# Kernel optimization log

Hardware: AMD Instinct MI355X
Metric: run time of the kernel (lower is better)

## Reference

```python
import jax, jax.numpy as jnp
import numpy as np

B, S, D = 2, 2048, 2048
H, HK, HD = 16, 4, 128          # query heads, kv heads, head dim (H*HD == D)
HID = 4 * D                      # SwiGLU hidden (mult=4)
WIN, SINK = 1024, 4              # sliding window, attention sink tokens
EPS = 1e-6
ROPE_BASE = 10000.0


def rmsnorm(x, g):
    return x * jax.lax.rsqrt(jnp.mean(x * x, axis=-1, keepdims=True) + EPS) * g


def rope_tables(seq_len, head_dim):
    inv = 1.0 / (ROPE_BASE ** (jnp.arange(0, head_dim, 2, dtype=jnp.float32) / head_dim))
    ang = jnp.arange(seq_len, dtype=jnp.float32)[:, None] * inv[None, :]  # [S, HD/2]
    return jnp.cos(ang), jnp.sin(ang)


def apply_rope(x, cos, sin):
    # x: [B, S, h, HD]; rotate-half convention
    x1, x2 = jnp.split(x, 2, axis=-1)
    c = cos[None, :, None, :]
    s = sin[None, :, None, :]
    return jnp.concatenate([x1 * c - x2 * s, x2 * c + x1 * s], axis=-1)


def setup_inputs() -> dict:
    key = jax.random.key(0)
    ks = jax.random.split(key, 10)
    p = 0.02
    return {
        "x": jax.random.normal(ks[0], (B, S, D), dtype=jnp.float32),
        "g1": jnp.ones((D,), dtype=jnp.float32),
        "g2": jnp.ones((D,), dtype=jnp.float32),
        "wq": jax.random.normal(ks[1], (D, H * HD), dtype=jnp.float32) * p,
        "wk": jax.random.normal(ks[2], (D, HK * HD), dtype=jnp.float32) * p,
        "wv": jax.random.normal(ks[3], (D, HK * HD), dtype=jnp.float32) * p,
        "wo": jax.random.normal(ks[4], (H * HD, D), dtype=jnp.float32) * p,
        "w_gate": jax.random.normal(ks[5], (D, HID), dtype=jnp.float32) * p,
        "w_up": jax.random.normal(ks[6], (D, HID), dtype=jnp.float32) * p,
        "w_down": jax.random.normal(ks[7], (HID, D), dtype=jnp.float32) * p,
    }


def reference(x, g1, g2, wq, wk, wv, wo, w_gate, w_up, w_down):
    # ---- pre-norm attention ----
    h = rmsnorm(x, g1)
    q = (h @ wq).reshape(B, S, H, HD)
    k = (h @ wk).reshape(B, S, HK, HD)
    v = (h @ wv).reshape(B, S, HK, HD)

    cos, sin = rope_tables(S, HD)
    q = apply_rope(q, cos, sin)
    k = apply_rope(k, cos, sin)

    # GQA: expand kv heads to query heads
    rep = H // HK
    k = jnp.repeat(k, rep, axis=2)  # [B, S, H, HD]
    v = jnp.repeat(v, rep, axis=2)

    scores = jnp.einsum("bqhd,bkhd->bhqk", q, k) / jnp.sqrt(jnp.float32(HD))

    # causal + sliding-window + attention-sink mask
    i = jnp.arange(S)[:, None]
    j = jnp.arange(S)[None, :]
    allowed = (j <= i) & (((i - j) < WIN) | (j < SINK))  # [S, S]
    scores = jnp.where(allowed[None, None], scores, jnp.float32(-1e9))

    attn = jax.nn.softmax(scores, axis=-1)
    a = jnp.einsum("bhqk,bkhd->bqhd", attn, v).reshape(B, S, H * HD) @ wo

    x = x + a

    # ---- pre-norm SwiGLU FFN ----
    h2 = rmsnorm(x, g2)
    ffn = (jax.nn.silu(h2 @ w_gate) * (h2 @ w_up)) @ w_down
    return x + ffn
```

## Files before the change

### kernel.cpp

```cpp
#include <hip/hip_runtime.h>
#include <hip/hip_bf16.h>
#include <stdint.h>

#define TOK 4096
#define SEQ 2048
#define DM 2048
#define NH 16
#define NKV 4
#define HDIM 128
#define HID 8192
#define WIN 1024
#define SINKN 4

typedef float f32x4 __attribute__((ext_vector_type(4)));
typedef __bf16 bf16x8 __attribute__((ext_vector_type(8)));
typedef unsigned short u16;
typedef unsigned int u32;

#define VM(n) asm volatile("s_waitcnt vmcnt(" #n ")" ::: "memory")
#define LGKM0 asm volatile("s_waitcnt lgkmcnt(0)" ::: "memory")

__device__ __forceinline__ u16 f2bf(float f) {
  union { float f; u32 u; } v; v.f = f;
  return (u16)((v.u + 0x7fffu + ((v.u >> 16) & 1u)) >> 16);
}
__device__ __forceinline__ float bf2f(u16 h) {
  union { u32 u; float f; } v; v.u = ((u32)h) << 16;
  return v.f;
}
__device__ __forceinline__ f32x4 mfma16(bf16x8 a, bf16x8 b, f32x4 c) {
  return __builtin_amdgcn_mfma_f32_16x16x32_bf16(a, b, c, 0, 0, 0);
}
__device__ __forceinline__ void gld16(const u16* g, u16* l) {
  __builtin_amdgcn_global_load_lds(
      (const __attribute__((address_space(1))) u32*)g,
      (__attribute__((address_space(3))) u32*)l, 16, 0, 0);
}
__device__ __forceinline__ void bar() {
  asm volatile("s_barrier" ::: "memory");
}
__device__ __forceinline__ void swz_rc(int c, int& row, int& k8) {
  row = 2 * (c >> 3) + (((c >> 2) & 1) ^ ((c >> 4) & 1));
  k8 = (c & 3) ^ (row & 3);
}
__device__ __forceinline__ void raster8(int wg, int nwg, int nbx, int& bx, int& by) {
  int cpx = nwg >> 3;
  int s = (wg & 7) * cpx + (wg >> 3);
  by = 8 * (s / (8 * nbx)) + (s & 7);
  bx = (s >> 3) % nbx;
}

__global__ __launch_bounds__(256)
void wtrans(const float* __restrict__ in, u16* __restrict__ out, int K, int N)
{
  __shared__ float t[32][33];
  int tx = threadIdx.x & 31, ty = threadIdx.x >> 5;
  int bx = blockIdx.x, by = blockIdx.y;
  #pragma unroll
  for (int i = 0; i < 4; i++) {
    int r = ty + i * 8;
    t[r][tx] = in[(size_t)(by * 32 + r) * N + bx * 32 + tx];
  }
  __syncthreads();
  #pragma unroll
  for (int i = 0; i < 4; i++) {
    int r = ty + i * 8;
    out[(size_t)(bx * 32 + r) * K + by * 32 + tx] = f2bf(t[tx][r]);
  }
}

__global__ __launch_bounds__(256)
void vtrans(const u16* __restrict__ in, int ld, u16* __restrict__ out)
{
  __shared__ u16 t[32][33];
  int tx = threadIdx.x & 31, ty = threadIdx.x >> 5;
  int bx = blockIdx.x;
  int by = blockIdx.y;
  #pragma unroll
  for (int i = 0; i < 4; i++) {
    int r = ty + i * 8;
    t[r][tx] = in[(size_t)(by * 32 + r) * ld + bx * 32 + tx];
  }
  __syncthreads();
  int b = (by * 32) >> 11;
  int s0 = (by * 32) & (SEQ - 1);
  #pragma unroll
  for (int i = 0; i < 4; i++) {
    int c = bx * 32 + ty + i * 8;
    out[(size_t)(b * (NKV * HDIM) + c) * SEQ + s0 + tx] = t[tx][ty + i * 8];
  }
}

__global__ __launch_bounds__(256)
void rope_table_k(float* __restrict__ ct, float* __restrict__ st)
{
  int idx = blockIdx.x * 256 + threadIdx.x;
  int pos = idx >> 6, d = idx & 63;
  float inv = powf(10000.0f, -(float)d / 64.0f);
  float a = (float)pos * inv;
  ct[idx] = cosf(a);
  st[idx] = sinf(a);
}

__global__ void rope_apply_k(u16* __restrict__ q, int ld,
                             const float* __restrict__ ct,
                             const float* __restrict__ st, float scale)
{
  int t = blockIdx.x;
  int hh = threadIdx.x >> 6;
  int d = threadIdx.x & 63;
  int pos = t & (SEQ - 1);
  size_t base = (size_t)t * ld + hh * HDIM + d;
  float x1 = bf2f(q[base]), x2 = bf2f(q[base + 64]);
  float c = ct[pos * 64 + d], s = st[pos * 64 + d];
  q[base]      = f2bf((x1 * c - x2 * s) * scale);
  q[base + 64] = f2bf((x2 * c + x1 * s) * scale);
}

__global__ __launch_bounds__(256)
void rmsnorm_k(const float* __restrict__ x, const float* __restrict__ g,
               u16* __restrict__ o)
{
  int row = blockIdx.x;
  int tid = threadIdx.x;
  const float* xr = x + (size_t)row * DM;
  float4 v0 = *(const float4*)(xr + tid * 8);
  float4 v1 = *(const float4*)(xr + tid * 8 + 4);
  float ss = v0.x*v0.x + v0.y*v0.y + v0.z*v0.z + v0.w*v0.w
           + v1.x*v1.x + v1.y*v1.y + v1.z*v1.z + v1.w*v1.w;
  #pragma unroll
  for (int d = 1; d < 64; d <<= 1) ss += __shfl_xor(ss, d);
  __shared__ float red[4];
  if ((tid & 63) == 0) red[tid >> 6] = ss;
  __syncthreads();
  float inv = rsqrtf((red[0] + red[1] + red[2] + red[3]) * (1.0f / DM) + 1e-6f);
  float4 g0 = *(const float4*)(g + tid * 8);
  float4 g1 = *(const float4*)(g + tid * 8 + 4);
  ushort4 o0, o1;
  o0.x = f2bf(v0.x * inv * g0.x); o0.y = f2bf(v0.y * inv * g0.y);
  o0.z = f2bf(v0.z * inv * g0.z); o0.w = f2bf(v0.w * inv * g0.w);
  o1.x = f2bf(v1.x * inv * g1.x); o1.y = f2bf(v1.y * inv * g1.y);
  o1.z = f2bf(v1.z * inv * g1.z); o1.w = f2bf(v1.w * inv * g1.w);
  *(ushort4*)(o + (size_t)row * DM + tid * 8) = o0;
  *(ushort4*)(o + (size_t)row * DM + tid * 8 + 4) = o1;
}

template<int EPI, int GU>
__global__ __launch_bounds__(512, 1)
void gemmp(const u16* __restrict__ A, const u16* __restrict__ Bt,
           const u16* __restrict__ Bu, u16* __restrict__ Cb,
           float* __restrict__ Cf, const float* __restrict__ X,
           int M, int N, int K, int nbx)
{
  constexpr int ASZ = 128 * 64;
  constexpr int SLOT = ASZ + 256 * 64;
  __shared__ u16 lds[3 * SLOT];

  int bx, by;
  raster8(blockIdx.x, gridDim.x, nbx, bx, by);
  int m0 = by * 128;
  int n0 = bx * (GU ? 128 : 256);

  int tid = threadIdx.x;
  int l = tid & 63, w = tid >> 6;
  int l16 = l & 15, lg = l >> 4;
  int wr = w >> 2, wc = w & 3;

  int aoff[4][2], boff[4][2];
  #pragma unroll
  for (int m = 0; m < 4; m++)
    #pragma unroll
    for (int kk = 0; kk < 2; kk++) {
      int row = wr * 64 + m * 16 + l16;
      aoff[m][kk] = ((row * 128 + kk * 64 + lg * 16) ^ ((row & 7) << 4)) >> 1;
    }
  #pragma unroll
  for (int n = 0; n < 4; n++)
    #pragma unroll
    for (int kk = 0; kk < 2; kk++) {
      int br = GU ? ((n >> 1) * 128 + wc * 32 + (n & 1) * 16 + l16)
                  : (wc * 64 + n * 16 + l16);
      boff[n][kk] = ASZ + (((br * 128 + kk * 64 + lg * 16) ^ ((br & 7) << 4)) >> 1);
    }

  int urow = tid >> 3;
  int cc = (tid & 7) ^ (urow & 7);
  const u16* pA[2];
  const u16* pB[4];
  pA[0] = A + (size_t)(m0 + urow) * K + cc * 8;
  pA[1] = A + (size_t)(m0 + 64 + urow) * K + cc * 8;
  #pragma unroll
  for (int u = 0; u < 4; u++) {
    if (GU) pB[u] = (u < 2 ? Bt + (size_t)(n0 + u * 64 + urow) * K
                           : Bu + (size_t)(n0 + (u - 2) * 64 + urow) * K) + cc * 8;
    else    pB[u] = Bt + (size_t)(n0 + u * 64 + urow) * K + cc * 8;
  }

  const int NT = K >> 6;

  auto stA = [&](int tt, int u) {
    gld16(pA[u] + (size_t)tt * 64, lds + (tt % 3) * SLOT + u * 4096 + tid * 8);
  };
  auto stB = [&](int tt, int u) {
    gld16(pB[u] + (size_t)tt * 64, lds + (tt % 3) * SLOT + ASZ + u * 4096 + tid * 8);
  };

  #pragma unroll
  for (int u = 0; u < 4; u++) stB(0, u);
  stA(0, 0); stA(0, 1);
  #pragma unroll
  for (int u = 0; u < 4; u++) stB(1, u);
  stA(1, 0); stA(1, 1);
  VM(6);
  bar();

  f32x4 acc[4][4];
  f32x4 zero = {0.f, 0.f, 0.f, 0.f};
  #pragma unroll
  for (int m = 0; m < 4; m++)
    #pragma unroll
    for (int n = 0; n < 4; n++) acc[m][n] = zero;

  for (int t = 0; t < NT; ++t) {
    u16* cur = lds + (t % 3) * SLOT;
    const bool st = (t + 2 < NT);

    if (st) { stB(t + 2, 0); stB(t + 2, 1); stB(t + 2, 2); }
    bf16x8 a[4][2], b[2][2];
    #pragma unroll
    for (int m = 0; m < 4; m++) {
      a[m][0] = *(const bf16x8*)(cur + aoff[m][0]);
      a[m][1] = *(const bf16x8*)(cur + aoff[m][1]);
    }
    #pragma unroll
    for (int n = 0; n < 2; n++) {
      b[n][0] = *(const bf16x8*)(cur + boff[n][0]);
      b[n][1] = *(const bf16x8*)(cur + boff[n][1]);
    }
    bar();
    LGKM0;
    __builtin_amdgcn_sched_barrier(0);
    __builtin_amdgcn_s_setprio(1);
    #pragma unroll
    for (int m = 0; m < 4; m++)
      #pragma unroll
      for (int n = 0; n < 2; n++) {
        acc[m][n] = mfma16(a[m][0], b[n][0], acc[m][n]);
        acc[m][n] = mfma16(a[m][1], b[n][1], acc[m][n]);
      }
    __builtin_amdgcn_s_setprio(0);
    __builtin_amdgcn_sched_barrier(0);
    bar();

    if (st) { stB(t + 2, 3); stA(t + 2, 0); stA(t + 2, 1); }
    bf16x8 c2[2][2];
    #pragma unroll
    for (int n = 0; n < 2; n++) {
      c2[n][0] = *(const bf16x8*)(cur + boff[n + 2][0]);
      c2[n][1] = *(const bf16x8*)(cur + boff[n + 2][1]);
    }
    if (st) { VM(6); }
    else if (t + 1 < NT) { VM(0); }
    bar();
    LGKM0;
    __builtin_amdgcn_sched_barrier(0);
    __builtin_amdgcn_s_setprio(1);
    #pragma unroll
    for (int m = 0; m < 4; m++)
      #pragma unroll
      for (int n = 0; n < 2; n++) {
        acc[m][n + 2] = mfma16(a[m][0], c2[n][0], acc[m][n + 2]);
        acc[m][n + 2] = mfma16(a[m][1], c2[n][1], acc[m][n + 2]);
      }
    __builtin_amdgcn_s_setprio(0);
    __builtin_amdgcn_sched_barrier(0);
    bar();
  }

  if (GU) {
    #pragma unroll
    for (int m = 0; m < 4; m++) {
      int row = m0 + wr * 64 + m * 16 + lg * 4;
      #pragma unroll
      for (int n = 0; n < 2; n++) {
        int col = n0 + wc * 32 + n * 16 + l16;
        #pragma unroll
        for (int r = 0; r < 4; r++) {
          float gt = acc[m][n][r];
          float up = acc[m][n + 2][r];
          float sg = gt / (1.0f + __expf(-gt));
          Cb[(size_t)(row + r) * N + col] = f2bf(sg * up);
        }
      }
    }
  } else {
    #pragma unroll
    for (int m = 0; m < 4; m++) {
      int row = m0 + wr * 64 + m * 16 + lg * 4;
      #pragma unroll
      for (int n = 0; n < 4; n++) {
        int col = n0 + wc * 64 + n * 16 + l16;
        #pragma unroll
        for (int r = 0; r < 4; r++) {
          size_t idx = (size_t)(row + r) * N + col;
          float v = acc[m][n][r];
          if (EPI == 0) {
            Cb[idx] = f2bf(v);
          } else if (EPI == 1) {
            Cf[idx] = X[idx] + v;
          } else {
            Cf[idx] += v;
          }
        }
      }
    }
  }
}

__global__ __launch_bounds__(256)
void attn_k(const u16* __restrict__ qb, int ldq,
            const u16* __restrict__ kb, int ldk,
            const u16* __restrict__ vbt, u16* __restrict__ ao)
{
  int q0 = blockIdx.x * 128;
  int h = blockIdx.y;
  int b = blockIdx.z;
  int hk = h >> 2;
  int tid = threadIdx.x;
  int w = tid >> 6, l = tid & 63;
  int l16 = l & 15, lg = l >> 4;

  __shared__ u16 Ks[32 * 128];
  __shared__ u16 Vt[128 * 32];
  __shared__ u16 Ps[4][32 * 40];
  u16* Pw = Ps[w];

  bf16x8 qf[2][4];
  #pragma unroll
  for (int m = 0; m < 2; m++)
    #pragma unroll
    for (int kd = 0; kd < 4; kd++) {
      int row = q0 + w * 32 + m * 16 + l16;
      qf[m][kd] = *(const bf16x8*)(qb + (size_t)(b * SEQ + row) * ldq
                                   + h * HDIM + kd * 32 + lg * 8);
    }

  f32x4 oacc[2][8];
  float mrun[2][4], lrun[2][4];
  f32x4 zero = {0.f, 0.f, 0.f, 0.f};
  #pragma unroll
  for (int m = 0; m < 2; m++) {
    #pragma unroll
    for (int nd = 0; nd < 8; nd++) oacc[m][nd] = zero;
    #pragma unroll
    for (int r = 0; r < 4; r++) { mrun[m][r] = -1e9f; lrun[m][r] = 0.f; }
  }

  int kr0 = tid >> 4,        kc0 = (tid & 15) ^ (kr0 & 7);
  int kr1 = (tid + 256) >> 4, kc1 = (tid & 15) ^ (kr1 & 7);
  int vd0, vk0, vd1, vk1;
  swz_rc(tid, vd0, vk0);
  swz_rc(tid + 256, vd1, vk1);
  const u16* kbase = kb + (size_t)(b * SEQ) * ldk + hk * HDIM;
  const u16* vbase = vbt + (size_t)(b * NKV + hk) * HDIM * SEQ;

  int koff[2][4];
  #pragma unroll
  for (int n = 0; n < 2; n++)
    #pragma unroll
    for (int kd = 0; kd < 4; kd++) {
      int key = n * 16 + l16;
      koff[n][kd] = ((key * 128) + kd * 32 + lg * 8) ^ ((key & 7) * 8);
    }
  int voff[8];
  #pragma unroll
  for (int nd = 0; nd < 8; nd++) {
    int d = nd * 16 + l16;
    voff[nd] = (d * 32 + lg * 8) ^ ((d & 7) * 8);
  }

  int lo = (q0 >= WIN) ? ((q0 - (WIN - 1)) >> 5) : 0;
  int hi = (q0 + 127) >> 5;

  for (int it = (lo > 0 ? lo - 1 : 0); it <= hi; ++it) {
    int kt = (it < lo) ? 0 : it;
    gld16(kbase + (size_t)(kt * 32 + kr0) * ldk + kc0 * 8, Ks + tid * 8);
    gld16(kbase + (size_t)(kt * 32 + kr1) * ldk + kc1 * 8, Ks + (tid + 256) * 8);
    gld16(vbase + (size_t)vd0 * SEQ + kt * 32 + vk0 * 8, Vt + tid * 8);
    gld16(vbase + (size_t)vd1 * SEQ + kt * 32 + vk1 * 8, Vt + (tid + 256) * 8);
    __syncthreads();

    f32x4 sacc[2][2];
    sacc[0][0] = zero; sacc[0][1] = zero; sacc[1][0] = zero; sacc[1][1] = zero;
    #pragma unroll
    for (int kd = 0; kd < 4; kd++) {
      bf16x8 kf0 = *(const bf16x8*)(Ks + koff[0][kd]);
      bf16x8 kf1 = *(const bf16x8*)(Ks + koff[1][kd]);
      #pragma unroll
      for (int m = 0; m < 2; m++) {
        sacc[m][0] = mfma16(qf[m][kd], kf0, sacc[m][0]);
        sacc[m][1] = mfma16(qf[m][kd], kf1, sacc[m][1]);
      }
    }

    #pragma unroll
    for (int m = 0; m < 2; m++) {
      float sc[4];
      #pragma unroll
      for (int r = 0; r < 4; r++) {
        int i = q0 + w * 32 + m * 16 + lg * 4 + r;
        int j0 = kt * 32 + l16;
        int j1 = j0 + 16;
        float s0 = sacc[m][0][r];
        float s1 = sacc[m][1][r];
        bool ok0 = (j0 <= i) && ((i - j0 < WIN) || (j0 < SINKN));
        bool ok1 = (j1 <= i) && ((i - j1 < WIN) || (j1 < SINKN));
        s0 = ok0 ? s0 : -1e9f;
        s1 = ok1 ? s1 : -1e9f;
        float mx = fmaxf(s0, s1);
        mx = fmaxf(mx, __shfl_xor(mx, 1));
        mx = fmaxf(mx, __shfl_xor(mx, 2));
        mx = fmaxf(mx, __shfl_xor(mx, 4));
        mx = fmaxf(mx, __shfl_xor(mx, 8));
        float mold = mrun[m][r];
        float mnew = fmaxf(mold, mx);
        float scl = __expf(mold - mnew);
        mrun[m][r] = mnew;
        float p0 = __expf(s0 - mnew);
        float p1 = __expf(s1 - mnew);
        int prow = m * 16 + lg * 4 + r;
        Pw[prow * 40 + l16] = f2bf(p0);
        Pw[prow * 40 + 16 + l16] = f2bf(p1);
        float ps = p0 + p1;
        ps += __shfl_xor(ps, 1);
        ps += __shfl_xor(ps, 2);
        ps += __shfl_xor(ps, 4);
        ps += __shfl_xor(ps, 8);
        lrun[m][r] = lrun[m][r] * scl + ps;
        sc[r] = scl;
      }
      #pragma unroll
      for (int nd = 0; nd < 8; nd++) {
        oacc[m][nd][0] *= sc[0];
        oacc[m][nd][1] *= sc[1];
        oacc[m][nd][2] *= sc[2];
        oacc[m][nd][3] *= sc[3];
      }
    }

    bf16x8 pa0 = *(const bf16x8*)(Pw + l16 * 40 + lg * 8);
    bf16x8 pa1 = *(const bf16x8*)(Pw + (16 + l16) * 40 + lg * 8);
    #pragma unroll
    for (int nd = 0; nd < 8; nd++) {
      bf16x8 vf = *(const bf16x8*)(Vt + voff[nd]);
      oacc[0][nd] = mfma16(pa0, vf, oacc[0][nd]);
      oacc[1][nd] = mfma16(pa1, vf, oacc[1][nd]);
    }
    __syncthreads();
  }

  #pragma unroll
  for (int m = 0; m < 2; m++)
    #pragma unroll
    for (int r = 0; r < 4; r++) {
      float invl = 1.0f / lrun[m][r];
      int row = q0 + w * 32 + m * 16 + lg * 4 + r;
      #pragma unroll
      for (int nd = 0; nd < 8; nd++) {
        int col = nd * 16 + l16;
        ao[(size_t)(b * SEQ + row) * (NH * HDIM) + h * HDIM + col] =
            f2bf(oacc[m][nd][r] * invl);
      }
    }
}

extern "C" void kernel_launch(void* const* d_in, const int* in_sizes, int n_in,
                              void* d_out, int out_size, void* d_ws, size_t ws_size,
                              hipStream_t stream)
{
  (void)in_sizes; (void)n_in; (void)out_size;
  const float* x  = (const float*)d_in[0];
  const float* g1 = (const float*)d_in[1];
  const float* g2 = (const float*)d_in[2];
  const float* wq = (const float*)d_in[3];
  const float* wk = (const float*)d_in[4];
  const float* wv = (const float*)d_in[5];
  const float* wo = (const float*)d_in[6];
  const float* wg = (const float*)d_in[7];
  const float* wu = (const float*)d_in[8];
  const float* wd = (const float*)d_in[9];
  float* out = (float*)d_out;

  char* ws = (char*)d_ws;
  size_t off = 0;
  auto alloc = [&](size_t bytes) {
    char* p = ws + off;
    off += (bytes + 255) & ~(size_t)255;
    return p;
  };
  const int NQKV = 3072;
  u16* wqkv_t = (u16*)alloc((size_t)NQKV * DM * 2);
  u16* wo_t   = (u16*)alloc((size_t)DM * DM * 2);
  u16* wg_t   = (u16*)alloc((size_t)HID * DM * 2);
  u16* wu_t   = (u16*)alloc((size_t)HID * DM * 2);
  u16* wd_t   = (u16*)alloc((size_t)DM * HID * 2);
  u16* hb     = (u16*)alloc((size_t)TOK * DM * 2);
  char* span0 = ws + off;
  u16* qkvb   = (u16*)alloc((size_t)TOK * NQKV * 2);
  u16* vbt    = (u16*)alloc((size_t)TOK * NKV * HDIM * 2);
  u16* aob    = (u16*)alloc((size_t)TOK * NH * HDIM * 2);
  size_t span_used = (size_t)(ws + off - span0);
  size_t gu_need = (size_t)TOK * HID * 2;
  if (gu_need > span_used) alloc(gu_need - span_used);
  u16* gu = (u16*)span0;
  float* ct  = (float*)alloc((size_t)SEQ * 64 * 4);
  float* st  = (float*)alloc((size_t)SEQ * 64 * 4);
  if (off > ws_size) return;

  dim3 blk(256);
  dim3 blk512(512);

  wtrans<<<dim3(DM / 32, DM / 32), blk, 0, stream>>>(wq, wqkv_t, DM, DM);
  wtrans<<<dim3((NKV * HDIM) / 32, DM / 32), blk, 0, stream>>>(wk, wqkv_t + (size_t)DM * DM, DM, NKV * HDIM);
  wtrans<<<dim3((NKV * HDIM) / 32, DM / 32), blk, 0, stream>>>(wv, wqkv_t + (size_t)(DM + NKV * HDIM) * DM, DM, NKV * HDIM);
  wtrans<<<dim3(DM / 32, DM / 32), blk, 0, stream>>>(wo, wo_t, DM, DM);
  wtrans<<<dim3(HID / 32, DM / 32), blk, 0, stream>>>(wg, wg_t, DM, HID);
  wtrans<<<dim3(HID / 32, DM / 32), blk, 0, stream>>>(wu, wu_t, DM, HID);
  wtrans<<<dim3(DM / 32, HID / 32), blk, 0, stream>>>(wd, wd_t, HID, DM);

  rope_table_k<<<SEQ * 64 / 256, blk, 0, stream>>>(ct, st);
  rmsnorm_k<<<TOK, blk, 0, stream>>>(x, g1, hb);

  gemmp<0, 0><<<dim3((NQKV / 256) * (TOK / 128)), blk512, 0, stream>>>(
      hb, wqkv_t, nullptr, qkvb, nullptr, nullptr, TOK, NQKV, DM, NQKV / 256);

  rope_apply_k<<<TOK, dim3(NH * 64), 0, stream>>>(qkvb, NQKV, ct, st, 0.08838834764831845f);
  rope_apply_k<<<TOK, dim3(NKV * 64), 0, stream>>>(qkvb + DM, NQKV, ct, st, 1.0f);
  vtrans<<<dim3((NKV * HDIM) / 32, TOK / 32), blk, 0, stream>>>(qkvb + DM + NKV * HDIM, NQKV, vbt);

  attn_k<<<dim3(SEQ / 128, NH, 2), blk, 0, stream>>>(qkvb, NQKV, qkvb + DM, NQKV, vbt, aob);

  gemmp<1, 0><<<dim3((DM / 256) * (TOK / 128)), blk512, 0, stream>>>(
      aob, wo_t, nullptr, nullptr, out, x, TOK, DM, DM, DM / 256);
  rmsnorm_k<<<TOK, blk, 0, stream>>>(out, g2, hb);

  gemmp<0, 1><<<dim3((HID / 128) * (TOK / 128)), blk512, 0, stream>>>(
      hb, wg_t, wu_t, gu, nullptr, nullptr, TOK, HID, DM, HID / 128);

  gemmp<3, 0><<<dim3((DM / 256) * (TOK / 128)), blk512, 0, stream>>>(
      gu, wd_t, nullptr, nullptr, out, nullptr, TOK, DM, HID, DM / 256);
}
```

Baseline: 821.9 us.

## Add 256x256 gate/up GEMM kernel and overlap B-fragment LDS reads

```diff
diff --git a/kernel.cpp b/kernel.cpp
--- a/kernel.cpp
+++ b/kernel.cpp
@@ -18,7 +18,8 @@
 typedef unsigned int u32;
 
 #define VM(n) asm volatile("s_waitcnt vmcnt(" #n ")" ::: "memory")
-#define LGKM0 asm volatile("s_waitcnt lgkmcnt(0)" ::: "memory")
+#define LG(n) asm volatile("s_waitcnt lgkmcnt(" #n ")" ::: "memory")
+#define SCHED0 __builtin_amdgcn_sched_barrier(0)
 
 __device__ __forceinline__ u16 f2bf(float f) {
   union { float f; u32 u; } v; v.f = f;
@@ -145,12 +146,11 @@
   *(ushort4*)(o + (size_t)row * DM + tid * 8 + 4) = o1;
 }
 
-template<int EPI, int GU>
+template<int EPI>
 __global__ __launch_bounds__(512, 1)
 void gemmp(const u16* __restrict__ A, const u16* __restrict__ Bt,
-           const u16* __restrict__ Bu, u16* __restrict__ Cb,
-           float* __restrict__ Cf, const float* __restrict__ X,
-           int M, int N, int K, int nbx)
+           u16* __restrict__ Cb, float* __restrict__ Cf,
+           const float* __restrict__ X, int M, int N, int K, int nbx)
 {
   constexpr int ASZ = 128 * 64;
   constexpr int SLOT = ASZ + 256 * 64;
@@ -159,7 +159,7 @@
   int bx, by;
   raster8(blockIdx.x, gridDim.x, nbx, bx, by);
   int m0 = by * 128;
-  int n0 = bx * (GU ? 128 : 256);
+  int n0 = bx * 256;
 
   int tid = threadIdx.x;
   int l = tid & 63, w = tid >> 6;
@@ -178,8 +178,7 @@
   for (int n = 0; n < 4; n++)
     #pragma unroll
     for (int kk = 0; kk < 2; kk++) {
-      int br = GU ? ((n >> 1) * 128 + wc * 32 + (n & 1) * 16 + l16)
-                  : (wc * 64 + n * 16 + l16);
+      int br = wc * 64 + n * 16 + l16;
       boff[n][kk] = ASZ + (((br * 128 + kk * 64 + lg * 16) ^ ((br & 7) << 4)) >> 1);
     }
 
@@ -190,11 +189,8 @@
   pA[0] = A + (size_t)(m0 + urow) * K + cc * 8;
   pA[1] = A + (size_t)(m0 + 64 + urow) * K + cc * 8;
   #pragma unroll
-  for (int u = 0; u < 4; u++) {
-    if (GU) pB[u] = (u < 2 ? Bt + (size_t)(n0 + u * 64 + urow) * K
-                           : Bu + (size_t)(n0 + (u - 2) * 64 + urow) * K) + cc * 8;
-    else    pB[u] = Bt + (size_t)(n0 + u * 64 + urow) * K + cc * 8;
-  }
+  for (int u = 0; u < 4; u++)
+    pB[u] = Bt + (size_t)(n0 + u * 64 + urow) * K + cc * 8;
 
   const int NT = K >> 6;
 
@@ -226,7 +222,7 @@
     const bool st = (t + 2 < NT);
 
     if (st) { stB(t + 2, 0); stB(t + 2, 1); stB(t + 2, 2); }
-    bf16x8 a[4][2], b[2][2];
+    bf16x8 a[4][2], b[2][2], c2[2][2];
     #pragma unroll
     for (int m = 0; m < 4; m++) {
       a[m][0] = *(const bf16x8*)(cur + aoff[m][0]);
@@ -237,9 +233,15 @@
       b[n][0] = *(const bf16x8*)(cur + boff[n][0]);
       b[n][1] = *(const bf16x8*)(cur + boff[n][1]);
     }
-    bar();
-    LGKM0;
-    __builtin_amdgcn_sched_barrier(0);
+    SCHED0;
+    #pragma unroll
+    for (int n = 0; n < 2; n++) {
+      c2[n][0] = *(const bf16x8*)(cur + boff[n + 2][0]);
+      c2[n][1] = *(const bf16x8*)(cur + boff[n + 2][1]);
+    }
+    bar();
+    LG(4);
+    SCHED0;
     __builtin_amdgcn_s_setprio(1);
     #pragma unroll
     for (int m = 0; m < 4; m++)
@@ -249,21 +251,15 @@
         acc[m][n] = mfma16(a[m][1], b[n][1], acc[m][n]);
       }
     __builtin_amdgcn_s_setprio(0);
-    __builtin_amdgcn_sched_barrier(0);
+    SCHED0;
     bar();
 
     if (st) { stB(t + 2, 3); stA(t + 2, 0); stA(t + 2, 1); }
-    bf16x8 c2[2][2];
-    #pragma unroll
-    for (int n = 0; n < 2; n++) {
-      c2[n][0] = *(const bf16x8*)(cur + boff[n + 2][0]);
-      c2[n][1] = *(const bf16x8*)(cur + boff[n + 2][1]);
-    }
     if (st) { VM(6); }
     else if (t + 1 < NT) { VM(0); }
     bar();
-    LGKM0;
-    __builtin_amdgcn_sched_barrier(0);
+    LG(0);
+    SCHED0;
     __builtin_amdgcn_s_setprio(1);
     #pragma unroll
     for (int m = 0; m < 4; m++)
@@ -273,45 +269,197 @@
         acc[m][n + 2] = mfma16(a[m][1], c2[n][1], acc[m][n + 2]);
       }
     __builtin_amdgcn_s_setprio(0);
-    __builtin_amdgcn_sched_barrier(0);
-    bar();
-  }
-
-  if (GU) {
-    #pragma unroll
-    for (int m = 0; m < 4; m++) {
-      int row = m0 + wr * 64 + m * 16 + lg * 4;
-      #pragma unroll
-      for (int n = 0; n < 2; n++) {
-        int col = n0 + wc * 32 + n * 16 + l16;
-        #pragma unroll
-        for (int r = 0; r < 4; r++) {
-          float gt = acc[m][n][r];
-          float up = acc[m][n + 2][r];
-          float sg = gt / (1.0f + __expf(-gt));
-          Cb[(size_t)(row + r) * N + col] = f2bf(sg * up);
+    SCHED0;
+    bar();
+  }
+
+  #pragma unroll
+  for (int m = 0; m < 4; m++) {
+    int row = m0 + wr * 64 + m * 16 + lg * 4;
+    #pragma unroll
+    for (int n = 0; n < 4; n++) {
+      int col = n0 + wc * 64 + n * 16 + l16;
+      #pragma unroll
+      for (int r = 0; r < 4; r++) {
+        size_t idx = (size_t)(row + r) * N + col;
+        float v = acc[m][n][r];
+        if (EPI == 0) {
+          Cb[idx] = f2bf(v);
+        } else if (EPI == 1) {
+          Cf[idx] = X[idx] + v;
+        } else {
+          Cf[idx] += v;
         }
       }
     }
-  } else {
-    #pragma unroll
-    for (int m = 0; m < 4; m++) {
-      int row = m0 + wr * 64 + m * 16 + lg * 4;
-      #pragma unroll
-      for (int n = 0; n < 4; n++) {
-        int col = n0 + wc * 64 + n * 16 + l16;
-        #pragma unroll
-        for (int r = 0; r < 4; r++) {
-          size_t idx = (size_t)(row + r) * N + col;
-          float v = acc[m][n][r];
-          if (EPI == 0) {
-            Cb[idx] = f2bf(v);
-          } else if (EPI == 1) {
-            Cf[idx] = X[idx] + v;
-          } else {
-            Cf[idx] += v;
-          }
-        }
+  }
+}
+
+__global__ __launch_bounds__(512, 1)
+void gemm256gu(const u16* __restrict__ A, const u16* __restrict__ Bg,
+               const u16* __restrict__ Bu, u16* __restrict__ Gu,
+               int K, int nbx)
+{
+  constexpr int SLOT = 32768;
+  __shared__ u16 lds[2 * SLOT];
+
+  int bx, by;
+  raster8(blockIdx.x, gridDim.x, nbx, bx, by);
+  int m0 = by * 256, n0 = bx * 128;
+
+  int tid = threadIdx.x;
+  int l = tid & 63, w = tid >> 6;
+  int l16 = l & 15, lg = l >> 4;
+  int wr = w >> 2, wc = w & 3;
+
+  int sw = (l16 & 7) << 4;
+  int aoffk[2], boffk[2];
+  #pragma unroll
+  for (int kk = 0; kk < 2; kk++) {
+    aoffk[kk] = ((wr * 128 + l16) * 128 + ((kk * 64 + lg * 16) ^ sw)) >> 1;
+    boffk[kk] = 16384 + ((((wc * 32 + l16) * 128) + ((kk * 64 + lg * 16) ^ sw)) >> 1);
+  }
+
+  int rh = tid >> 3;
+  int cc = (tid & 7) ^ (rh & 7);
+  const u16* pA0[2]; const u16* pA1[2]; const u16* pBg[2]; const u16* pBu[2];
+  #pragma unroll
+  for (int ll = 0; ll < 2; ll++) {
+    pA0[ll] = A + (size_t)(m0 + ll * 64 + rh) * K + cc * 8;
+    pA1[ll] = A + (size_t)(m0 + 128 + ll * 64 + rh) * K + cc * 8;
+    pBg[ll] = Bg + (size_t)(n0 + ll * 64 + rh) * K + cc * 8;
+    pBu[ll] = Bu + (size_t)(n0 + ll * 64 + rh) * K + cc * 8;
+  }
+
+  const int NT = K >> 6;
+
+  auto stA0 = [&](int tt) {
+    u16* d = lds + (tt & 1) * SLOT;
+    gld16(pA0[0] + (size_t)tt * 64, d + tid * 8);
+    gld16(pA0[1] + (size_t)tt * 64, d + 4096 + tid * 8);
+  };
+  auto stA1 = [&](int tt) {
+    u16* d = lds + (tt & 1) * SLOT + 8192;
+    gld16(pA1[0] + (size_t)tt * 64, d + tid * 8);
+    gld16(pA1[1] + (size_t)tt * 64, d + 4096 + tid * 8);
+  };
+  auto stBg = [&](int tt) {
+    u16* d = lds + (tt & 1) * SLOT + 16384;
+    gld16(pBg[0] + (size_t)tt * 64, d + tid * 8);
+    gld16(pBg[1] + (size_t)tt * 64, d + 4096 + tid * 8);
+  };
+  auto stBu = [&](int tt) {
+    u16* d = lds + (tt & 1) * SLOT + 16384 + 8192;
+    gld16(pBu[0] + (size_t)tt * 64, d + tid * 8);
+    gld16(pBu[1] + (size_t)tt * 64, d + 4096 + tid * 8);
+  };
+
+  stA0(0); stA1(0); stBg(0); stBu(0);
+  stA0(1); stBg(1); stBu(1);
+  VM(6);
+  bar();
+
+  f32x4 acc[8][4];
+  f32x4 zero = {0.f, 0.f, 0.f, 0.f};
+  #pragma unroll
+  for (int m = 0; m < 8; m++)
+    #pragma unroll
+    for (int n = 0; n < 4; n++) acc[m][n] = zero;
+
+  for (int t = 0; t < NT; ++t) {
+    u16* cur = lds + (t & 1) * SLOT;
+
+    if (t + 1 < NT) stA1(t + 1);
+    bf16x8 a0[4], a1[4], b0[4];
+    #pragma unroll
+    for (int m = 0; m < 4; m++)
+      a0[m] = *(const bf16x8*)(cur + aoffk[0] + m * 1024);
+    #pragma unroll
+    for (int n = 0; n < 4; n++)
+      b0[n] = *(const bf16x8*)(cur + boffk[0] + (n & 1) * 1024 + (n >> 1) * 8192);
+    SCHED0;
+    #pragma unroll
+    for (int m = 0; m < 4; m++)
+      a1[m] = *(const bf16x8*)(cur + aoffk[0] + 4096 + m * 1024);
+    bar();
+    LG(4);
+    SCHED0;
+    __builtin_amdgcn_s_setprio(1);
+    #pragma unroll
+    for (int m = 0; m < 4; m++)
+      #pragma unroll
+      for (int n = 0; n < 4; n++)
+        acc[m][n] = mfma16(a0[m], b0[n], acc[m][n]);
+    __builtin_amdgcn_s_setprio(0);
+    SCHED0;
+    bar();
+
+    bf16x8 a2[4], b1[4];
+    #pragma unroll
+    for (int m = 0; m < 4; m++)
+      a2[m] = *(const bf16x8*)(cur + aoffk[1] + m * 1024);
+    #pragma unroll
+    for (int n = 0; n < 4; n++)
+      b1[n] = *(const bf16x8*)(cur + boffk[1] + (n & 1) * 1024 + (n >> 1) * 8192);
+    bar();
+    LG(8);
+    SCHED0;
+    __builtin_amdgcn_s_setprio(1);
+    #pragma unroll
+    for (int m = 0; m < 4; m++)
+      #pragma unroll
+      for (int n = 0; n < 4; n++)
+        acc[4 + m][n] = mfma16(a1[m], b0[n], acc[4 + m][n]);
+    __builtin_amdgcn_s_setprio(0);
+    SCHED0;
+    bar();
+
+    bf16x8 a3[4];
+    #pragma unroll
+    for (int m = 0; m < 4; m++)
+      a3[m] = *(const bf16x8*)(cur + aoffk[1] + 4096 + m * 1024);
+    bar();
+    LG(4);
+    SCHED0;
+    __builtin_amdgcn_s_setprio(1);
+    #pragma unroll
+    for (int m = 0; m < 4; m++)
+      #pragma unroll
+      for (int n = 0; n < 4; n++)
+        acc[m][n] = mfma16(a2[m], b1[n], acc[m][n]);
+    __builtin_amdgcn_s_setprio(0);
+    SCHED0;
+    bar();
+
+    if (t + 2 < NT) { stA0(t + 2); stBg(t + 2); stBu(t + 2); }
+    bar();
+    LG(0);
+    SCHED0;
+    __builtin_amdgcn_s_setprio(1);
+    #pragma unroll
+    for (int m = 0; m < 4; m++)
+      #pragma unroll
+      for (int n = 0; n < 4; n++)
+        acc[4 + m][n] = mfma16(a3[m], b1[n], acc[4 + m][n]);
+    __builtin_amdgcn_s_setprio(0);
+    SCHED0;
+    if (t + 2 < NT) { VM(6); }
+    else if (t + 1 < NT) { VM(0); }
+    bar();
+  }
+
+  #pragma unroll
+  for (int m = 0; m < 8; m++) {
+    int row = m0 + wr * 128 + m * 16 + lg * 4;
+    #pragma unroll
+    for (int n = 0; n < 2; n++) {
+      int col = n0 + wc * 32 + n * 16 + l16;
+      #pragma unroll
+      for (int r = 0; r < 4; r++) {
+        float gt = acc[m][n][r];
+        float up = acc[m][n + 2][r];
+        float sg = gt / (1.0f + __expf(-gt));
+        Gu[(size_t)(row + r) * HID + col] = f2bf(sg * up);
       }
     }
   }
@@ -531,8 +679,8 @@
   rope_table_k<<<SEQ * 64 / 256, blk, 0, stream>>>(ct, st);
   rmsnorm_k<<<TOK, blk, 0, stream>>>(x, g1, hb);
 
-  gemmp<0, 0><<<dim3((NQKV / 256) * (TOK / 128)), blk512, 0, stream>>>(
-      hb, wqkv_t, nullptr, qkvb, nullptr, nullptr, TOK, NQKV, DM, NQKV / 256);
+  gemmp<0><<<dim3((NQKV / 256) * (TOK / 128)), blk512, 0, stream>>>(
+      hb, wqkv_t, qkvb, nullptr, nullptr, TOK, NQKV, DM, NQKV / 256);
 
   rope_apply_k<<<TOK, dim3(NH * 64), 0, stream>>>(qkvb, NQKV, ct, st, 0.08838834764831845f);
   rope_apply_k<<<TOK, dim3(NKV * 64), 0, stream>>>(qkvb + DM, NQKV, ct, st, 1.0f);
@@ -540,13 +688,13 @@
 
   attn_k<<<dim3(SEQ / 128, NH, 2), blk, 0, stream>>>(qkvb, NQKV, qkvb + DM, NQKV, vbt, aob);
 
-  gemmp<1, 0><<<dim3((DM / 256) * (TOK / 128)), blk512, 0, stream>>>(
-      aob, wo_t, nullptr, nullptr, out, x, TOK, DM, DM, DM / 256);
+  gemmp<1><<<dim3((DM / 256) * (TOK / 128)), blk512, 0, stream>>>(
+      aob, wo_t, nullptr, out, x, TOK, DM, DM, DM / 256);
   rmsnorm_k<<<TOK, blk, 0, stream>>>(out, g2, hb);
 
-  gemmp<0, 1><<<dim3((HID / 128) * (TOK / 128)), blk512, 0, stream>>>(
-      hb, wg_t, wu_t, gu, nullptr, nullptr, TOK, HID, DM, HID / 128);
-
-  gemmp<3, 0><<<dim3((DM / 256) * (TOK / 128)), blk512, 0, stream>>>(
-      gu, wd_t, nullptr, nullptr, out, nullptr, TOK, DM, HID, DM / 256);
-}
+  gemm256gu<<<dim3((HID / 128) * (TOK / 256)), blk512, 0, stream>>>(
+      hb, wg_t, wu_t, gu, DM, HID / 128);
+
+  gemmp<3><<<dim3((DM / 256) * (TOK / 128)), blk512, 0, stream>>>(
+      gu, wd_t, nullptr, out, nullptr, TOK, DM, HID, DM / 256);
+}
```

After: 796.4 us. 1.03x faster.
